# Optimization experiments

Hardware: AMD Instinct MI355X
Metric: run time of the kernel (lower is better)

The kernel has to match this reference:

```python
import jax, jax.numpy as jnp
import numpy as np

N_EL, N_NB, DIM = 8192, 24, 256
CUTOFF = 5.0
F0, F1 = 32, 16
N_ENV = 8
N_FEAT = 4  # [dist, dx, dy, dz]


def setup_inputs() -> dict:
    key = jax.random.key(0)
    ks = jax.random.split(key, 24)
    d = {}
    d['elec'] = jax.random.normal(ks[0], (N_EL, DIM), jnp.float32)
    d['msg'] = jax.random.normal(ks[1], (N_EL, DIM), jnp.float32)
    # positions inside a box of half the cutoff so pairs are within range
    d['r'] = jax.random.uniform(ks[2], (N_EL, 3), jnp.float32) * (0.5 * CUTOFF)
    d['r_nb'] = jax.random.uniform(ks[3], (N_EL, N_NB, 3), jnp.float32) * (0.5 * CUTOFF)
    d['s'] = jax.random.randint(ks[4], (N_EL,), 0, 2, jnp.int32)
    d['s_nb'] = jax.random.randint(ks[5], (N_EL, N_NB), 0, 2, jnp.int32)
    d['hinit_nb'] = jax.random.normal(ks[6], (N_EL, N_NB, DIM), jnp.float32)
    # parameters
    def lecun(k, shape):
        fan_in = shape[0]
        return jax.random.normal(k, shape, jnp.float32) / np.float32(np.sqrt(fan_in))
    d['W_in'] = lecun(ks[7], (DIM, DIM)); d['b_in'] = jnp.zeros((DIM,), jnp.float32)
    d['ee_scales'] = jax.random.uniform(ks[8], (N_ENV,), jnp.float32, 0.5, CUTOFF)
    d['ee_kernel'] = lecun(ks[9], (N_FEAT, F0))
    d['ee_bias'] = 2.0 * jax.random.normal(ks[10], (F0,), jnp.float32)
    d['Wf'] = lecun(ks[11], (F0 + N_ENV, F1)); d['bf'] = jnp.zeros((F1,), jnp.float32)
    d['Wsame'] = lecun(ks[12], (F1, DIM))
    d['Wdiff'] = lecun(ks[13], (F1, DIM))
    d['W1'] = lecun(ks[14], (DIM, DIM)); d['b1'] = jnp.zeros((DIM,), jnp.float32)
    d['W2'] = lecun(ks[15], (DIM, DIM)); d['b2'] = jnp.zeros((DIM,), jnp.float32)
    d['W3'] = lecun(ks[16], (DIM, DIM)); d['b3'] = jnp.zeros((DIM,), jnp.float32)
    d['scale'] = jnp.float32(1.0)  # FixedScalingFactor (identity at init)
    return d


def _forward(elec, msg, r, r_nb, s, s_nb, hinit_nb,
             W_in, b_in, ee_scales, ee_kernel, ee_bias, Wf, bf,
             Wsame, Wdiff, W1, b1, W2, b2, W3, b3, scale):
    silu = jax.nn.silu
    elec1 = silu(elec @ W_in + b_in)                       # [N, D]
    # get_diff_features: [dist, dx, dy, dz]
    diff = r_nb - r[:, None, :]                             # [N, K, 3]
    dist = jnp.sqrt(jnp.sum(diff * diff, -1) + 1e-12)       # [N, K]
    feats = jnp.concatenate([dist[..., None], diff], -1)    # [N, K, 4]
    spin_mask = s[:, None] == s_nb                          # [N, K]
    # PairwiseFilter: MLP on diff-features + radial envelopes, smooth cutoff
    env = jnp.exp(-jnp.square(dist[..., None] / ee_scales)) # [N, K, E]
    h = silu(feats @ ee_kernel + ee_bias)                   # [N, K, F0]
    h = jnp.concatenate([h, env], -1)                       # [N, K, F0+E]
    x = dist / CUTOFF
    cut = jnp.where(dist < CUTOFF, jnp.square(1.0 - x) * (1.0 + 2.0 * x), 0.0)
    beta = (h @ Wf + bf) * cut[..., None]                   # [N, K, F1]
    gamma = jnp.where(spin_mask[..., None], beta @ Wsame, beta @ Wdiff)  # [N, K, D]
    hinit_msg = jnp.einsum('nid,nid->nd', silu(elec1[:, None] + hinit_nb), gamma)
    out = silu(elec1 @ W1 + b1 + hinit_msg)
    out = silu(out @ W2 + b2 + msg)
    out = silu(out @ W3 + b3)
    return (out + elec1) * scale


def reference(elec, msg, r, r_nb, s, s_nb, hinit_nb,
              W_in, b_in, ee_scales, ee_kernel, ee_bias, Wf, bf,
              Wsame, Wdiff, W1, b1, W2, b2, W3, b3, scale):
    return _forward(elec, msg, r, r_nb, s, s_nb, hinit_nb,
                    W_in, b_in, ee_scales, ee_kernel, ee_bias, Wf, bf,
                    Wsame, Wdiff, W1, b1, W2, b2, W3, b3, scale)
```

## Files before the change

kernel.cpp:

```cpp
#include <hip/hip_runtime.h>

#define DIM 256
#define PDIM 260
#define PD2  264
#define SBPITCH 20
#define NNB 24
#define NEL 8192
#define ROWS 16
#define NT 512
#define CUTOFF 5.0f

typedef unsigned int u32;
typedef unsigned short u16;
typedef __attribute__((ext_vector_type(8))) short bf16x8;
typedef __attribute__((ext_vector_type(4))) float f32x4;

__device__ __forceinline__ u16 f2b(float f){
  union{float f;u32 i;}v; v.f=f;
  u32 r = v.i + 0x7fffu + ((v.i>>16)&1u);
  return (u16)(r>>16);
}
__device__ __forceinline__ float b2f(u16 u){
  union{u32 i;float f;}v; v.i = ((u32)u)<<16; return v.f;
}
__device__ __forceinline__ float fast_silu(float x){
  float e = __builtin_amdgcn_exp2f(-1.44269504088896340f * x);
  return x * __builtin_amdgcn_rcpf(1.0f + e);
}

__global__ __launch_bounds__(256)
void wprep(const float* __restrict__ W0, const float* __restrict__ W1,
           const float* __restrict__ W2, const float* __restrict__ W3,
           const float* __restrict__ Wsame, const float* __restrict__ Wdiff,
           u16* __restrict__ ws){
  if (blockIdx.x < 1024){
    const int mat = blockIdx.x >> 8;
    const int n   = blockIdx.x & 255;
    const int k   = threadIdx.x;
    const float* W = (mat==0)?W0:(mat==1)?W1:(mat==2)?W2:W3;
    ws[(mat<<16) + (n<<8) + k] = f2b(W[(k<<8) + n]);
  } else {
    const int n = threadIdx.x;
    u16* dst = ws + 4*65536 + n*32;
    #pragma unroll
    for (int kk = 0; kk < 16; kk++){
      dst[kk]    = f2b(Wsame[kk*DIM + n]);
      dst[16+kk] = f2b(Wdiff[kk*DIM + n]);
    }
  }
}

template<int MODE, int ABF16>
__device__ __forceinline__ void gemm_mfma(
    const void* A, u16* sE1b, float* sR1,
    const u16* __restrict__ Wt, const float* __restrict__ bias,
    const float* __restrict__ extraGbl, float* __restrict__ outGbl,
    float scl, int n0, int t)
{
  const int lane = t & 63;
  const int ln   = lane & 15;
  const int quad = lane >> 4;
  const int nt0  = (t >> 6) << 1;
  f32x4 acc0 = {0.f,0.f,0.f,0.f};
  f32x4 acc1 = {0.f,0.f,0.f,0.f};
  const u16* bp0 = Wt + (nt0*16 + ln)*DIM;
  const u16* bp1 = bp0 + 16*DIM;
  #pragma unroll
  for (int ks = 0; ks < 8; ks++){
    const int k0 = ks*32 + quad*8;
    bf16x8 af;
    if (ABF16){
      af = *(const bf16x8*)((const u16*)A + ln*PD2 + k0);
    } else {
      const float* arow = (const float*)A + ln*PDIM;
      float4 a01 = *(const float4*)(arow + k0);
      float4 a23 = *(const float4*)(arow + k0 + 4);
      af[0]=(short)f2b(a01.x); af[1]=(short)f2b(a01.y);
      af[2]=(short)f2b(a01.z); af[3]=(short)f2b(a01.w);
      af[4]=(short)f2b(a23.x); af[5]=(short)f2b(a23.y);
      af[6]=(short)f2b(a23.z); af[7]=(short)f2b(a23.w);
    }
    bf16x8 b0 = *(const bf16x8*)(bp0 + k0);
    bf16x8 b1 = *(const bf16x8*)(bp1 + k0);
    acc0 = __builtin_amdgcn_mfma_f32_16x16x32_bf16(af, b0, acc0, 0, 0, 0);
    acc1 = __builtin_amdgcn_mfma_f32_16x16x32_bf16(af, b1, acc1, 0, 0, 0);
  }
  if (MODE == 2) __syncthreads();
  #pragma unroll
  for (int r = 0; r < 4; r++){
    const int m = quad*4 + r;
    #pragma unroll
    for (int tt = 0; tt < 2; tt++){
      const int n = (nt0+tt)*16 + ln;
      float v = (tt ? acc1[r] : acc0[r]) + bias[n];
      if (MODE == 1) v += sR1[m*PDIM + n];
      if (MODE == 2) v += extraGbl[(size_t)(n0+m)*DIM + n];
      v = fast_silu(v);
      if (MODE == 0)      sE1b[m*PD2 + n] = f2b(v);
      else if (MODE == 3) outGbl[(size_t)(n0+m)*DIM + n] = (v + b2f(sE1b[m*PD2 + n])) * scl;
      else                sR1[m*PDIM + n] = v;
    }
  }
}

__global__ __launch_bounds__(NT, 4)
void fused_moon_kernel(
    const float* __restrict__ elec, const float* __restrict__ msg,
    const float* __restrict__ rpos, const float* __restrict__ rnb,
    const int* __restrict__ s,    const int* __restrict__ snb,
    const float* __restrict__ hinit,
    const float* __restrict__ bin,
    const float* __restrict__ eesc, const float* __restrict__ eek,
    const float* __restrict__ eeb,  const float* __restrict__ Wf,
    const float* __restrict__ bfb,
    const float* __restrict__ b1, const float* __restrict__ b2,
    const float* __restrict__ b3,
    const float* __restrict__ scalep,
    const u16* __restrict__ Wt,
    float* __restrict__ out)
{
  __shared__ float sR1[ROWS*PDIM];
  __shared__ u16   sE1b[ROWS*PD2];
  __shared__ u16   sBC[NNB*16*SBPITCH];
  __shared__ u32   sMaskB[ROWS];
  const int t  = threadIdx.x;
  const int n0 = blockIdx.x * ROWS;

  if (t < ROWS) sMaskB[t] = 0u;
  {
    const float4* ep = (const float4*)elec;
    #pragma unroll
    for (int h = 0; h < 2; h++){
      const int idx = t + h*NT;
      float4 v = ep[(size_t)n0*64 + idx];
      *(float4*)&sR1[(idx>>6)*PDIM + (idx&63)*4] = v;
    }
  }
  __syncthreads();

  gemm_mfma<0,0>(sR1, sE1b, sR1, Wt, bin, nullptr, nullptr, 0.f, n0, t);

  if (t < ROWS*NNB) {
    const int rr = t / NNB;
    const int k  = t - rr*NNB;
    const int n  = n0 + rr;
    const float* rp  = rpos + n*3;
    const float* rnp = rnb + (n*NNB + k)*3;
    float dx = rnp[0] - rp[0];
    float dy = rnp[1] - rp[1];
    float dz = rnp[2] - rp[2];
    float dist = sqrtf(dx*dx + dy*dy + dz*dz + 1e-12f);
    float feats[4] = {dist, dx, dy, dz};
    float h[32];
    #pragma unroll
    for (int f4 = 0; f4 < 8; f4++){
      float4 a4 = *(const float4*)&eeb[4*f4];
      float av[4] = {a4.x, a4.y, a4.z, a4.w};
      #pragma unroll
      for (int i = 0; i < 4; i++){
        float4 kv = *(const float4*)&eek[i*32 + 4*f4];
        av[0]+=feats[i]*kv.x; av[1]+=feats[i]*kv.y; av[2]+=feats[i]*kv.z; av[3]+=feats[i]*kv.w;
      }
      h[4*f4+0]=fast_silu(av[0]); h[4*f4+1]=fast_silu(av[1]);
      h[4*f4+2]=fast_silu(av[2]); h[4*f4+3]=fast_silu(av[3]);
    }
    float env[8];
    #pragma unroll
    for (int e = 0; e < 8; e++){
      float q = dist * __builtin_amdgcn_rcpf(eesc[e]);
      env[e] = __builtin_amdgcn_exp2f(-1.44269504088896340f * q * q);
    }
    float xx = dist * (1.0f/CUTOFF);
    float cut = (dist < CUTOFF) ? (1.0f-xx)*(1.0f-xx)*(1.0f+2.0f*xx) : 0.0f;
    u16* rowp = &sBC[(k*16 + rr)*SBPITCH];
    #pragma unroll
    for (int j4 = 0; j4 < 4; j4++){
      float4 a4 = *(const float4*)&bfb[4*j4];
      float av[4] = {a4.x, a4.y, a4.z, a4.w};
      #pragma unroll
      for (int f = 0; f < 40; f++){
        float val = (f < 32) ? h[f] : env[f-32];
        float4 wv = *(const float4*)&Wf[f*16 + 4*j4];
        av[0]+=val*wv.x; av[1]+=val*wv.y; av[2]+=val*wv.z; av[3]+=val*wv.w;
      }
      ushort4 bv;
      bv.x = f2b(av[0]*cut); bv.y = f2b(av[1]*cut);
      bv.z = f2b(av[2]*cut); bv.w = f2b(av[3]*cut);
      *(ushort4*)(rowp + 4*j4) = bv;
    }
    if (s[n] == snb[n*NNB + k]) atomicOr(&sMaskB[rr], 1u << k);
  }
  __syncthreads();

  {
    const int lane = t & 63;
    const int ln   = lane & 15;
    const int quad = lane >> 4;
    const int w    = t >> 6;
    const int C0   = w << 5;
    const int nA   = C0 + (quad << 2);
    const u16* Wcat = Wt + 4*65536;
    bf16x8 bs0 = *(const bf16x8*)(Wcat + (C0 + ln)*32 + quad*8);
    bf16x8 bs1 = *(const bf16x8*)(Wcat + (C0 + 16 + ln)*32 + quad*8);

    float e1A[4], e1B[4];
    {
      ushort4 ea = *(const ushort4*)&sE1b[ln*PD2 + nA];
      ushort4 eb = *(const ushort4*)&sE1b[ln*PD2 + nA + 16];
      e1A[0]=b2f(ea.x); e1A[1]=b2f(ea.y); e1A[2]=b2f(ea.z); e1A[3]=b2f(ea.w);
      e1B[0]=b2f(eb.x); e1B[1]=b2f(eb.y); e1B[2]=b2f(eb.z); e1B[3]=b2f(eb.w);
    }
    const u32 mb = sMaskB[ln];
    const float* hp = hinit + (size_t)(n0 + ln)*NNB*DIM + nA;
    float4 hA0 = *(const float4*)(hp + 0*DIM);
    float4 hB0 = *(const float4*)(hp + 0*DIM + 16);
    float4 hA1 = *(const float4*)(hp + 1*DIM);
    float4 hB1 = *(const float4*)(hp + 1*DIM + 16);
    float4 hA2 = *(const float4*)(hp + 2*DIM);
    float4 hB2 = *(const float4*)(hp + 2*DIM + 16);
    float hmA[4] = {0.f,0.f,0.f,0.f};
    float hmB[4] = {0.f,0.f,0.f,0.f};
    for (int k = 0; k < NNB; k++){
      const int kp = (k+3 < NNB) ? (k+3) : (NNB-1);
      float4 hA3 = *(const float4*)(hp + kp*DIM);
      float4 hB3 = *(const float4*)(hp + kp*DIM + 16);
      bf16x8 b8 = *(const bf16x8*)(&sBC[(k*16 + ln)*SBPITCH + (quad&1)*8]);
      const u16 km = (u16)((((u32)(quad>>1) ^ ((mb>>k)&1u)) != 0u) ? 0xFFFFu : 0u);
      bf16x8 af;
      #pragma unroll
      for (int j = 0; j < 8; j++) af[j] = (short)((u16)b8[j] & km);
      f32x4 z = {0.f,0.f,0.f,0.f};
      f32x4 g0 = __builtin_amdgcn_mfma_f32_16x16x32_bf16(bs0, af, z, 0, 0, 0);
      f32x4 g1 = __builtin_amdgcn_mfma_f32_16x16x32_bf16(bs1, af, z, 0, 0, 0);
      hmA[0] += fast_silu(e1A[0]+hA0.x)*g0[0];
      hmA[1] += fast_silu(e1A[1]+hA0.y)*g0[1];
      hmA[2] += fast_silu(e1A[2]+hA0.z)*g0[2];
      hmA[3] += fast_silu(e1A[3]+hA0.w)*g0[3];
      hmB[0] += fast_silu(e1B[0]+hB0.x)*g1[0];
      hmB[1] += fast_silu(e1B[1]+hB0.y)*g1[1];
      hmB[2] += fast_silu(e1B[2]+hB0.z)*g1[2];
      hmB[3] += fast_silu(e1B[3]+hB0.w)*g1[3];
      hA0=hA1; hA1=hA2; hA2=hA3;
      hB0=hB1; hB1=hB2; hB2=hB3;
    }
    *(float4*)&sR1[ln*PDIM + nA]      = make_float4(hmA[0],hmA[1],hmA[2],hmA[3]);
    *(float4*)&sR1[ln*PDIM + nA + 16] = make_float4(hmB[0],hmB[1],hmB[2],hmB[3]);
  }
  __syncthreads();

  const float scl = scalep[0];

  gemm_mfma<1,1>(sE1b, sE1b, sR1, Wt + (1<<16), b1, nullptr, nullptr, 0.f, n0, t);
  __syncthreads();
  gemm_mfma<2,0>(sR1, sE1b, sR1, Wt + (2<<16), b2, msg, nullptr, 0.f, n0, t);
  __syncthreads();
  gemm_mfma<3,0>(sR1, sE1b, sR1, Wt + (3<<16), b3, nullptr, out, scl, n0, t);
}

extern "C" void kernel_launch(void* const* d_in, const int* in_sizes, int n_in,
                              void* d_out, int out_size, void* d_ws, size_t ws_size,
                              hipStream_t stream) {
  (void)in_sizes; (void)n_in; (void)ws_size; (void)out_size;
  const float* elec  = (const float*)d_in[0];
  const float* msg   = (const float*)d_in[1];
  const float* rpos  = (const float*)d_in[2];
  const float* rnb   = (const float*)d_in[3];
  const int*   s     = (const int*)d_in[4];
  const int*   snb   = (const int*)d_in[5];
  const float* hinit = (const float*)d_in[6];
  const float* Win   = (const float*)d_in[7];
  const float* bin   = (const float*)d_in[8];
  const float* eesc  = (const float*)d_in[9];
  const float* eek   = (const float*)d_in[10];
  const float* eeb   = (const float*)d_in[11];
  const float* Wf    = (const float*)d_in[12];
  const float* bfb   = (const float*)d_in[13];
  const float* Wsame = (const float*)d_in[14];
  const float* Wdiff = (const float*)d_in[15];
  const float* W1    = (const float*)d_in[16];
  const float* b1    = (const float*)d_in[17];
  const float* W2    = (const float*)d_in[18];
  const float* b2    = (const float*)d_in[19];
  const float* W3    = (const float*)d_in[20];
  const float* b3    = (const float*)d_in[21];
  const float* scl   = (const float*)d_in[22];
  float* outp        = (float*)d_out;
  u16*   wt          = (u16*)d_ws;

  wprep<<<dim3(1025), dim3(256), 0, stream>>>(Win, W1, W2, W3, Wsame, Wdiff, wt);
  fused_moon_kernel<<<dim3(NEL/ROWS), dim3(NT), 0, stream>>>(
      elec, msg, rpos, rnb, s, snb, hinit,
      bin, eesc, eek, eeb, Wf, bfb,
      b1, b2, b3, scl, wt, outp);
}
```

Measured before the change: 368.7 us.

## Double block threads so each wave owns one 16-column tile

The block size goes from 512 to 1024 threads. Each wave now computes one 16-column MFMA tile instead of two in every GEMM and in the hinit message loop. The pairwise filter work is split across two threads per (row, neighbour) pair, and the hinit prefetch depth rises from 3 to 4 rows. The aim is more waves in flight to hide the global-memory latency of streaming hinit_nb, at the cost of more barrier participants, duplicated filter-MLP work per thread, and register pressure under the new launch bounds.

Result: slower. 377.5 us (+2.4%).

```diff
diff --git a/kernel.cpp b/kernel.cpp
--- a/kernel.cpp
+++ b/kernel.cpp
@@ -7,7 +7,7 @@
 #define NNB 24
 #define NEL 8192
 #define ROWS 16
-#define NT 512
+#define NT 1024
 #define CUTOFF 5.0f
 
 typedef unsigned int u32;
@@ -60,11 +60,9 @@
   const int lane = t & 63;
   const int ln   = lane & 15;
   const int quad = lane >> 4;
-  const int nt0  = (t >> 6) << 1;
-  f32x4 acc0 = {0.f,0.f,0.f,0.f};
-  f32x4 acc1 = {0.f,0.f,0.f,0.f};
-  const u16* bp0 = Wt + (nt0*16 + ln)*DIM;
-  const u16* bp1 = bp0 + 16*DIM;
+  const int w    = t >> 6;
+  f32x4 acc = {0.f,0.f,0.f,0.f};
+  const u16* bp = Wt + (w*16 + ln)*DIM;
   #pragma unroll
   for (int ks = 0; ks < 8; ks++){
     const int k0 = ks*32 + quad*8;
@@ -80,30 +78,25 @@
       af[4]=(short)f2b(a23.x); af[5]=(short)f2b(a23.y);
       af[6]=(short)f2b(a23.z); af[7]=(short)f2b(a23.w);
     }
-    bf16x8 b0 = *(const bf16x8*)(bp0 + k0);
-    bf16x8 b1 = *(const bf16x8*)(bp1 + k0);
-    acc0 = __builtin_amdgcn_mfma_f32_16x16x32_bf16(af, b0, acc0, 0, 0, 0);
-    acc1 = __builtin_amdgcn_mfma_f32_16x16x32_bf16(af, b1, acc1, 0, 0, 0);
+    bf16x8 b0 = *(const bf16x8*)(bp + k0);
+    acc = __builtin_amdgcn_mfma_f32_16x16x32_bf16(af, b0, acc, 0, 0, 0);
   }
   if (MODE == 2) __syncthreads();
   #pragma unroll
   for (int r = 0; r < 4; r++){
     const int m = quad*4 + r;
-    #pragma unroll
-    for (int tt = 0; tt < 2; tt++){
-      const int n = (nt0+tt)*16 + ln;
-      float v = (tt ? acc1[r] : acc0[r]) + bias[n];
-      if (MODE == 1) v += sR1[m*PDIM + n];
-      if (MODE == 2) v += extraGbl[(size_t)(n0+m)*DIM + n];
-      v = fast_silu(v);
-      if (MODE == 0)      sE1b[m*PD2 + n] = f2b(v);
-      else if (MODE == 3) outGbl[(size_t)(n0+m)*DIM + n] = (v + b2f(sE1b[m*PD2 + n])) * scl;
-      else                sR1[m*PDIM + n] = v;
-    }
-  }
-}
-
-__global__ __launch_bounds__(NT, 4)
+    const int n = w*16 + ln;
+    float v = acc[r] + bias[n];
+    if (MODE == 1) v += sR1[m*PDIM + n];
+    if (MODE == 2) v += extraGbl[(size_t)(n0+m)*DIM + n];
+    v = fast_silu(v);
+    if (MODE == 0)      sE1b[m*PD2 + n] = f2b(v);
+    else if (MODE == 3) outGbl[(size_t)(n0+m)*DIM + n] = (v + b2f(sE1b[m*PD2 + n])) * scl;
+    else                sR1[m*PDIM + n] = v;
+  }
+}
+
+__global__ __launch_bounds__(NT, 8)
 void fused_moon_kernel(
     const float* __restrict__ elec, const float* __restrict__ msg,
     const float* __restrict__ rpos, const float* __restrict__ rnb,
@@ -129,20 +122,18 @@
   if (t < ROWS) sMaskB[t] = 0u;
   {
     const float4* ep = (const float4*)elec;
-    #pragma unroll
-    for (int h = 0; h < 2; h++){
-      const int idx = t + h*NT;
-      float4 v = ep[(size_t)n0*64 + idx];
-      *(float4*)&sR1[(idx>>6)*PDIM + (idx&63)*4] = v;
-    }
+    float4 v = ep[(size_t)n0*64 + t];
+    *(float4*)&sR1[(t>>6)*PDIM + (t&63)*4] = v;
   }
   __syncthreads();
 
   gemm_mfma<0,0>(sR1, sE1b, sR1, Wt, bin, nullptr, nullptr, 0.f, n0, t);
 
-  if (t < ROWS*NNB) {
-    const int rr = t / NNB;
-    const int k  = t - rr*NNB;
+  if (t < 2*ROWS*NNB) {
+    const int half = t & 1;
+    const int pr = t >> 1;
+    const int rr = pr / NNB;
+    const int k  = pr - rr*NNB;
     const int n  = n0 + rr;
     const float* rp  = rpos + n*3;
     const float* rnp = rnb + (n*NNB + k)*3;
@@ -174,7 +165,8 @@
     float cut = (dist < CUTOFF) ? (1.0f-xx)*(1.0f-xx)*(1.0f+2.0f*xx) : 0.0f;
     u16* rowp = &sBC[(k*16 + rr)*SBPITCH];
     #pragma unroll
-    for (int j4 = 0; j4 < 4; j4++){
+    for (int jj = 0; jj < 2; jj++){
+      const int j4 = half*2 + jj;
       float4 a4 = *(const float4*)&bfb[4*j4];
       float av[4] = {a4.x, a4.y, a4.z, a4.w};
       #pragma unroll
@@ -188,7 +180,7 @@
       bv.z = f2b(av[2]*cut); bv.w = f2b(av[3]*cut);
       *(ushort4*)(rowp + 4*j4) = bv;
     }
-    if (s[n] == snb[n*NNB + k]) atomicOr(&sMaskB[rr], 1u << k);
+    if (half == 0 && s[n] == snb[n*NNB + k]) atomicOr(&sMaskB[rr], 1u << k);
   }
   __syncthreads();
 
@@ -197,33 +189,26 @@
     const int ln   = lane & 15;
     const int quad = lane >> 4;
     const int w    = t >> 6;
-    const int C0   = w << 5;
+    const int C0   = w << 4;
     const int nA   = C0 + (quad << 2);
     const u16* Wcat = Wt + 4*65536;
     bf16x8 bs0 = *(const bf16x8*)(Wcat + (C0 + ln)*32 + quad*8);
-    bf16x8 bs1 = *(const bf16x8*)(Wcat + (C0 + 16 + ln)*32 + quad*8);
-
-    float e1A[4], e1B[4];
+
+    float e1A[4];
     {
       ushort4 ea = *(const ushort4*)&sE1b[ln*PD2 + nA];
-      ushort4 eb = *(const ushort4*)&sE1b[ln*PD2 + nA + 16];
       e1A[0]=b2f(ea.x); e1A[1]=b2f(ea.y); e1A[2]=b2f(ea.z); e1A[3]=b2f(ea.w);
-      e1B[0]=b2f(eb.x); e1B[1]=b2f(eb.y); e1B[2]=b2f(eb.z); e1B[3]=b2f(eb.w);
     }
     const u32 mb = sMaskB[ln];
     const float* hp = hinit + (size_t)(n0 + ln)*NNB*DIM + nA;
-    float4 hA0 = *(const float4*)(hp + 0*DIM);
-    float4 hB0 = *(const float4*)(hp + 0*DIM + 16);
-    float4 hA1 = *(const float4*)(hp + 1*DIM);
-    float4 hB1 = *(const float4*)(hp + 1*DIM + 16);
-    float4 hA2 = *(const float4*)(hp + 2*DIM);
-    float4 hB2 = *(const float4*)(hp + 2*DIM + 16);
+    float4 h0 = *(const float4*)(hp + 0*DIM);
+    float4 h1 = *(const float4*)(hp + 1*DIM);
+    float4 h2 = *(const float4*)(hp + 2*DIM);
+    float4 h3 = *(const float4*)(hp + 3*DIM);
     float hmA[4] = {0.f,0.f,0.f,0.f};
-    float hmB[4] = {0.f,0.f,0.f,0.f};
     for (int k = 0; k < NNB; k++){
-      const int kp = (k+3 < NNB) ? (k+3) : (NNB-1);
-      float4 hA3 = *(const float4*)(hp + kp*DIM);
-      float4 hB3 = *(const float4*)(hp + kp*DIM + 16);
+      const int kp = (k+4 < NNB) ? (k+4) : (NNB-1);
+      float4 h4 = *(const float4*)(hp + kp*DIM);
       bf16x8 b8 = *(const bf16x8*)(&sBC[(k*16 + ln)*SBPITCH + (quad&1)*8]);
       const u16 km = (u16)((((u32)(quad>>1) ^ ((mb>>k)&1u)) != 0u) ? 0xFFFFu : 0u);
       bf16x8 af;
@@ -231,20 +216,13 @@
       for (int j = 0; j < 8; j++) af[j] = (short)((u16)b8[j] & km);
       f32x4 z = {0.f,0.f,0.f,0.f};
       f32x4 g0 = __builtin_amdgcn_mfma_f32_16x16x32_bf16(bs0, af, z, 0, 0, 0);
-      f32x4 g1 = __builtin_amdgcn_mfma_f32_16x16x32_bf16(bs1, af, z, 0, 0, 0);
-      hmA[0] += fast_silu(e1A[0]+hA0.x)*g0[0];
-      hmA[1] += fast_silu(e1A[1]+hA0.y)*g0[1];
-      hmA[2] += fast_silu(e1A[2]+hA0.z)*g0[2];
-      hmA[3] += fast_silu(e1A[3]+hA0.w)*g0[3];
-      hmB[0] += fast_silu(e1B[0]+hB0.x)*g1[0];
-      hmB[1] += fast_silu(e1B[1]+hB0.y)*g1[1];
-      hmB[2] += fast_silu(e1B[2]+hB0.z)*g1[2];
-      hmB[3] += fast_silu(e1B[3]+hB0.w)*g1[3];
-      hA0=hA1; hA1=hA2; hA2=hA3;
-      hB0=hB1; hB1=hB2; hB2=hB3;
-    }
-    *(float4*)&sR1[ln*PDIM + nA]      = make_float4(hmA[0],hmA[1],hmA[2],hmA[3]);
-    *(float4*)&sR1[ln*PDIM + nA + 16] = make_float4(hmB[0],hmB[1],hmB[2],hmB[3]);
+      hmA[0] += fast_silu(e1A[0]+h0.x)*g0[0];
+      hmA[1] += fast_silu(e1A[1]+h0.y)*g0[1];
+      hmA[2] += fast_silu(e1A[2]+h0.z)*g0[2];
+      hmA[3] += fast_silu(e1A[3]+h0.w)*g0[3];
+      h0=h1; h1=h2; h2=h3; h3=h4;
+    }
+    *(float4*)&sR1[ln*PDIM + nA] = make_float4(hmA[0],hmA[1],hmA[2],hmA[3]);
   }
   __syncthreads();
 
```

## Stream hinit neighbor rows via async global-to-LDS double buffering

Applied to the files above, without the earlier changes.

Replaces the register-rotated triple-buffered global loads of hinit_nb with async global_load_lds transfers into a per-wave double-buffered LDS region. The first two neighbor slices are issued at kernel start, so they overlap with the elec load, the first GEMM and the filter computation, and later slices are prefetched two steps ahead with explicit vmcnt waits. The aim is to hide the latency of the dominant hinit stream and to lower register pressure. The cost is 32 KB of extra LDS per block, which may reduce occupancy, and correctness now depends on hand-placed waitcnt counts and on LDS write ordering with no barrier between the async writes and the reads.

Measured after the change: 369.8 us. No clear change (+0.3%).

```diff
diff --git a/kernel.cpp b/kernel.cpp
--- a/kernel.cpp
+++ b/kernel.cpp
@@ -14,6 +14,10 @@
 typedef unsigned short u16;
 typedef __attribute__((ext_vector_type(8))) short bf16x8;
 typedef __attribute__((ext_vector_type(4))) float f32x4;
+
+#define GL_LDS(g, l) __builtin_amdgcn_global_load_lds( \
+    (const __attribute__((address_space(1))) void*)(g), \
+    (__attribute__((address_space(3))) void*)(l), 16, 0, 0)
 
 __device__ __forceinline__ u16 f2b(float f){
   union{float f;u32 i;}v; v.f=f;
@@ -123,8 +127,21 @@
   __shared__ u16   sE1b[ROWS*PD2];
   __shared__ u16   sBC[NNB*16*SBPITCH];
   __shared__ u32   sMaskB[ROWS];
+  __shared__ float sH[8][2][512];
   const int t  = threadIdx.x;
   const int n0 = blockIdx.x * ROWS;
+  const int lane = t & 63;
+  const int w    = t >> 6;
+  const int C0   = w << 5;
+
+  const float* hsrc = hinit
+      + (size_t)(n0 + (lane & 15)) * NNB * DIM + C0 + ((lane >> 4) << 2);
+  float* sHw0 = &sH[w][0][0];
+  float* sHw1 = &sH[w][1][0];
+  GL_LDS(hsrc + 0*DIM,      sHw0);
+  GL_LDS(hsrc + 0*DIM + 16, sHw0 + 256);
+  GL_LDS(hsrc + 1*DIM,      sHw1);
+  GL_LDS(hsrc + 1*DIM + 16, sHw1 + 256);
 
   if (t < ROWS) sMaskB[t] = 0u;
   {
@@ -193,11 +210,8 @@
   __syncthreads();
 
   {
-    const int lane = t & 63;
     const int ln   = lane & 15;
     const int quad = lane >> 4;
-    const int w    = t >> 6;
-    const int C0   = w << 5;
     const int nA   = C0 + (quad << 2);
     const u16* Wcat = Wt + 4*65536;
     bf16x8 bs0 = *(const bf16x8*)(Wcat + (C0 + ln)*32 + quad*8);
@@ -211,37 +225,35 @@
       e1B[0]=b2f(eb.x); e1B[1]=b2f(eb.y); e1B[2]=b2f(eb.z); e1B[3]=b2f(eb.w);
     }
     const u32 mb = sMaskB[ln];
-    const float* hp = hinit + (size_t)(n0 + ln)*NNB*DIM + nA;
-    float4 hA0 = *(const float4*)(hp + 0*DIM);
-    float4 hB0 = *(const float4*)(hp + 0*DIM + 16);
-    float4 hA1 = *(const float4*)(hp + 1*DIM);
-    float4 hB1 = *(const float4*)(hp + 1*DIM + 16);
-    float4 hA2 = *(const float4*)(hp + 2*DIM);
-    float4 hB2 = *(const float4*)(hp + 2*DIM + 16);
     float hmA[4] = {0.f,0.f,0.f,0.f};
     float hmB[4] = {0.f,0.f,0.f,0.f};
     for (int k = 0; k < NNB; k++){
-      const int kp = (k+3 < NNB) ? (k+3) : (NNB-1);
-      float4 hA3 = *(const float4*)(hp + kp*DIM);
-      float4 hB3 = *(const float4*)(hp + kp*DIM + 16);
+      if (k < NNB-1) { asm volatile("s_waitcnt vmcnt(2)" ::: "memory"); }
+      else           { asm volatile("s_waitcnt vmcnt(0)" ::: "memory"); }
+      float* sHw = (k & 1) ? sHw1 : sHw0;
+      float4 hv0 = *(const float4*)&sHw[lane*4];
+      float4 hv1 = *(const float4*)&sHw[256 + lane*4];
       bf16x8 b8 = *(const bf16x8*)(&sBC[(k*16 + ln)*SBPITCH + (quad&1)*8]);
       const u16 km = (u16)((((u32)(quad>>1) ^ ((mb>>k)&1u)) != 0u) ? 0xFFFFu : 0u);
       bf16x8 af;
       #pragma unroll
       for (int j = 0; j < 8; j++) af[j] = (short)((u16)b8[j] & km);
+      __builtin_amdgcn_sched_barrier(0);
+      if (k + 2 < NNB){
+        GL_LDS(hsrc + (size_t)(k+2)*DIM,      sHw);
+        GL_LDS(hsrc + (size_t)(k+2)*DIM + 16, sHw + 256);
+      }
       f32x4 z = {0.f,0.f,0.f,0.f};
       f32x4 g0 = __builtin_amdgcn_mfma_f32_16x16x32_bf16(bs0, af, z, 0, 0, 0);
       f32x4 g1 = __builtin_amdgcn_mfma_f32_16x16x32_bf16(bs1, af, z, 0, 0, 0);
-      hmA[0] += fast_silu(e1A[0]+hA0.x)*g0[0];
-      hmA[1] += fast_silu(e1A[1]+hA0.y)*g0[1];
-      hmA[2] += fast_silu(e1A[2]+hA0.z)*g0[2];
-      hmA[3] += fast_silu(e1A[3]+hA0.w)*g0[3];
-      hmB[0] += fast_silu(e1B[0]+hB0.x)*g1[0];
-      hmB[1] += fast_silu(e1B[1]+hB0.y)*g1[1];
-      hmB[2] += fast_silu(e1B[2]+hB0.z)*g1[2];
-      hmB[3] += fast_silu(e1B[3]+hB0.w)*g1[3];
-      hA0=hA1; hA1=hA2; hA2=hA3;
-      hB0=hB1; hB1=hB2; hB2=hB3;
+      hmA[0] += fast_silu(e1A[0]+hv0.x)*g0[0];
+      hmA[1] += fast_silu(e1A[1]+hv0.y)*g0[1];
+      hmA[2] += fast_silu(e1A[2]+hv0.z)*g0[2];
+      hmA[3] += fast_silu(e1A[3]+hv0.w)*g0[3];
+      hmB[0] += fast_silu(e1B[0]+hv1.x)*g1[0];
+      hmB[1] += fast_silu(e1B[1]+hv1.y)*g1[1];
+      hmB[2] += fast_silu(e1B[2]+hv1.z)*g1[2];
+      hmB[3] += fast_silu(e1B[3]+hv1.w)*g1[3];
     }
     *(float4*)&sR1[ln*PDIM + nA]      = make_float4(hmA[0],hmA[1],hmA[2],hmA[3]);
     *(float4*)&sR1[ln*PDIM + nA + 16] = make_float4(hmB[0],hmB[1],hmB[2],hmB[3]);
```
